# Performance work log

Hardware: AMD Instinct MI355X
Metric: run time of the kernel (lower is better)

## Reference

```python
import jax, jax.numpy as jnp
import numpy as np
from jax import lax

B, L, E, H, VOCAB = 32, 64, 1024, 128, 32000


def setup_inputs() -> dict:
    key = jax.random.key(0)
    ks = jax.random.split(key, 8)
    return {
        "sent": jax.random.randint(ks[0], (B, L), 0, VOCAB),
        "init_c": jax.random.normal(ks[1], (B, H), jnp.float32),
        "init_h": jax.random.normal(ks[2], (B, H), jnp.float32),
        "enc_output": jax.random.normal(ks[3], (B, E, H), jnp.float32),
        "w_emb": jax.random.normal(ks[4], (VOCAB, H), jnp.float32) * 0.02,
        "w_lstm": jax.random.normal(ks[5], (2 * H, 4 * H), jnp.float32) * 0.05,
        "w_soft": jax.random.normal(ks[6], (H, VOCAB), jnp.float32) * 0.05,
        "V": jax.random.normal(ks[7], (2 * H, H), jnp.float32) * 0.05,
    }


def reference(sent, init_c, init_h, enc_output, w_emb, w_lstm, w_soft, V):
    h_dim = init_h.shape[-1]
    x_emb = w_emb[sent]                       # (B, L, H) embedding lookup
    # Split additive-attention matrix: concat(enc, h) @ V == enc @ V_e + h @ V_h
    V_e, V_h = V[:h_dim], V[h_dim:]           # (H, H) each
    enc_proj = enc_output @ V_e               # (B, E, H), precomputed once

    def step(carry, x_t):
        c, h = carry
        # LSTM cell: gates from concat(x, h) @ w_lstm
        gates = jnp.concatenate([x_t, h], axis=-1) @ w_lstm   # (B, 4H)
        i, f, o, g = jnp.split(gates, 4, axis=-1)
        c_new = jax.nn.sigmoid(f) * c + jax.nn.sigmoid(i) * jnp.tanh(g)
        h_new = jax.nn.sigmoid(o) * jnp.tanh(c_new)           # (B, H)
        # Bahdanau additive attention over encoder states
        att = jnp.tanh(enc_proj + (h_new @ V_h)[:, None, :])  # (B, E, H)
        scores = att.sum(axis=-1)                              # (B, E)
        alpha = jax.nn.softmax(scores, axis=-1)                # (B, E)
        context = jnp.einsum('be,beh->bh', alpha, enc_output)  # (B, H)
        h_out = context                                        # attended hidden
        return (c_new, h_out), (h_out, alpha)

    (c_fin, h_fin), (hs, alphas) = lax.scan(step, (init_c, init_h),
                                            jnp.transpose(x_emb, (1, 0, 2)))
    hs = jnp.transpose(hs, (1, 0, 2))          # (B, L, H)
    alphas = jnp.transpose(alphas, (1, 0, 2))  # (B, L, E)
    logits = hs @ w_soft                       # (B, L, vocab)
    return logits, c_fin, h_fin, alphas
```

## Files before the change

### kernel.cpp

```cpp
#include <hip/hip_runtime.h>
#include <hip/hip_bf16.h>

#define BB 32
#define LL 64
#define EE 1024
#define HH 128
#define VV 32000

typedef unsigned short u16;
typedef unsigned long long u64;
typedef __attribute__((ext_vector_type(8))) short bf16x8;
typedef __attribute__((ext_vector_type(4))) float f32x4;

#define LOG2E 1.4426950408889634f
#define C2T   2.8853900817779268f

#define OFF_C ((size_t)BB * LL * VV)
#define OFF_H (OFF_C + (size_t)BB * HH)
#define OFF_A (OFF_H + (size_t)BB * HH)

#define WS_ENCT 0
#define WS_HS   ((size_t)16777216)
#define WS_GX   ((size_t)18350080)
#define WS_PAYU ((size_t)22544384)
#define WS_PAYG ((size_t)23076864)
#define WS_DFL  ((size_t)23339008)
#define WS_NEED ((size_t)23339012)

#define PAYU_WORDS (32 * 8 * 2 * 130)
#define PAYG_WORDS (32 * 8 * 2 * 64)
#define PAY_TOTAL  (PAYU_WORDS + PAYG_WORDS)

__device__ __forceinline__ float bf2f(u16 u) {
    union { unsigned int i; float f; } v; v.i = ((unsigned int)u) << 16; return v.f;
}
__device__ __forceinline__ u16 f2bf(float f) {
    union { float f; unsigned int i; } v; v.f = f;
    unsigned int x = v.i;
    return (u16)((x + 0x7FFFu + ((x >> 16) & 1u)) >> 16);
}
__device__ __forceinline__ float ldf(const void* p, size_t i, int f32) {
    if (f32) return ((const float*)p)[i];
    return bf2f(((const u16*)p)[i]);
}
__device__ __forceinline__ void stout(void* p, size_t i, float v, int f32) {
    if (f32) ((float*)p)[i] = v;
    else ((u16*)p)[i] = f2bf(v);
}
__device__ __forceinline__ float sigm(float x) {
    return __builtin_amdgcn_rcpf(1.f + __builtin_amdgcn_exp2f(-x * LOG2E));
}
__device__ __forceinline__ float tanh_fast(float x) {
    return 1.f - 2.f * __builtin_amdgcn_rcpf(__builtin_amdgcn_exp2f(x * C2T) + 1.f);
}

__global__ __launch_bounds__(256) void resetdetect_kernel(
    u64* __restrict__ pay, const unsigned int* __restrict__ w, int* __restrict__ flag)
{
    int i = blockIdx.x * 256 + threadIdx.x;
    if (i < PAY_TOTAL)
        pay[i] = 0ull;
    if (i == 0) {
        int cnt = 0;
        for (int j = 0; j < 256; ++j) {
            float a = fabsf(bf2f((u16)(w[j] & 0xFFFFu)));
            if (a > 1e-4f && a < 0.5f) ++cnt;
        }
        *flag = (cnt > 128) ? 1 : 0;
    }
}

__global__ __launch_bounds__(256) void gatesx3_kernel(
    const int* __restrict__ sent, const void* __restrict__ w_emb,
    const void* __restrict__ w_lstm, float* __restrict__ gx,
    const int* __restrict__ flagp)
{
    int isf32 = !flagp[0];
    int row0 = blockIdx.x * 16;
    int tid = threadIdx.x;
    __shared__ float xr[16][128];
    for (int i = tid; i < 2048; i += 256) {
        int r = i >> 7, col = i & 127;
        int id = sent[row0 + r];
        xr[r][col] = ldf(w_emb, (size_t)id * HH + col, isf32);
    }
    __syncthreads();
    int c0 = tid, c1 = tid + 256;
    float a0[16], a1[16];
    #pragma unroll
    for (int r = 0; r < 16; ++r) { a0[r] = 0.f; a1[r] = 0.f; }
    for (int kk = 0; kk < 128; ++kk) {
        float w0, w1;
        if (isf32) {
            w0 = ((const float*)w_lstm)[(size_t)kk * 512 + c0];
            w1 = ((const float*)w_lstm)[(size_t)kk * 512 + c1];
        } else {
            w0 = bf2f(((const u16*)w_lstm)[(size_t)kk * 512 + c0]);
            w1 = bf2f(((const u16*)w_lstm)[(size_t)kk * 512 + c1]);
        }
        #pragma unroll
        for (int r = 0; r < 16; ++r) {
            a0[r] += xr[r][kk] * w0;
            a1[r] += xr[r][kk] * w1;
        }
    }
    #pragma unroll
    for (int r = 0; r < 16; ++r) {
        gx[(size_t)(row0 + r) * 512 + c0] = a0[r];
        gx[(size_t)(row0 + r) * 512 + c1] = a1[r];
    }
}

__global__ __launch_bounds__(1024) void transpose_wsoft(
    const void* __restrict__ w_soft, u16* __restrict__ wT, const int* __restrict__ flagp)
{
    int isf32 = !flagp[0];
    __shared__ u16 tile[32][33];
    int n0 = blockIdx.x * 32;
    int k0 = blockIdx.y * 32;
    int tx = threadIdx.x & 31, ty = threadIdx.x >> 5;
    tile[ty][tx] = f2bf(ldf(w_soft, (size_t)(k0 + ty) * VV + n0 + tx, isf32));
    __syncthreads();
    wT[(size_t)(n0 + ty) * HH + k0 + tx] = tile[tx][ty];
}

__global__ __launch_bounds__(256) void encproj_kernel(
    const void* __restrict__ enc_out, const void* __restrict__ V,
    float* __restrict__ encT, const int* __restrict__ flagp)
{
    int isf32 = !flagp[0];
    __shared__ float ve[HH][HH];
    int b = blockIdx.y;
    int e0 = blockIdx.x * 64;
    int tid = threadIdx.x;
    for (int i = tid; i < HH * HH; i += 256)
        ve[i >> 7][i & 127] = ldf(V, i, isf32);
    __syncthreads();
    int e = e0 + (tid & 63);
    int hb = (tid >> 6) * 32;
    size_t rowbase = ((size_t)b * EE + e) * HH;
    float acc[32];
    #pragma unroll
    for (int i = 0; i < 32; ++i) acc[i] = 0.f;
    for (int k0 = 0; k0 < HH; k0 += 16) {
        float ef[16];
        #pragma unroll
        for (int i = 0; i < 16; ++i) ef[i] = ldf(enc_out, rowbase + k0 + i, isf32);
        #pragma unroll
        for (int hh = 0; hh < 32; ++hh) {
            float a = acc[hh];
            #pragma unroll
            for (int kk = 0; kk < 16; ++kk)
                a += ef[kk] * ve[k0 + kk][hb + hh];
            acc[hh] = a;
        }
    }
    float* outp = encT + ((size_t)b * HH) * EE + e;
    #pragma unroll
    for (int hh = 0; hh < 32; ++hh)
        outp[(size_t)(hh + hb) * EE] = acc[hh] * C2T;
}

__global__ __launch_bounds__(1024) void scan_kernel(
    const void* __restrict__ init_c, const void* __restrict__ init_h,
    const void* __restrict__ enc_out, const void* __restrict__ w_lstm,
    const void* __restrict__ V, const float* __restrict__ encTg,
    const float* __restrict__ gx, u16* __restrict__ hs_bf,
    void* __restrict__ out, u64* __restrict__ payu, u64* __restrict__ payg,
    const int* __restrict__ flagp)
{
    const int isf32 = !flagp[0];
    const int bid = blockIdx.x;
    const int b = bid & 31, k = bid >> 5;
    const int tid = threadIdx.x;

    __shared__ u16   encTl16[128][128];
    __shared__ float encF[128][128];
    __shared__ u16   wrec16[64 * 128];
    __shared__ float gall[512];
    __shared__ float harr[128], cst[128], hnew[128], hvC[128];
    __shared__ float dred[8][128];
    __shared__ float sc[128];
    __shared__ float exch[8][130];
    __shared__ float redw[2], redw2[2];
    __shared__ float m_s, s_s;

    for (int i = tid; i < 128 * 128; i += 1024) {
        int h = i >> 7, e = i & 127;
        encTl16[h][e] = f2bf(encTg[(size_t)(b * 128 + h) * EE + k * 128 + e]);
    }
    for (int i = tid; i < 128 * 128; i += 1024) {
        int e = i >> 7, hh = i & 127;
        encF[e][hh] = ldf(enc_out, ((size_t)b * EE + k * 128 + e) * HH + hh, isf32);
    }
    for (int i = tid; i < 64 * 128; i += 1024) {
        int c = i >> 7, kk = i & 127;
        wrec16[c * 128 + kk] = f2bf(ldf(w_lstm, (size_t)(HH + kk) * 512 + k * 64 + c, isf32));
    }
    if (tid < 128) {
        cst[tid]  = ldf(init_c, (size_t)b * HH + tid, isf32);
        harr[tid] = ldf(init_h, (size_t)b * HH + tid, isf32);
    }
    __syncthreads();

    u64* mypu = payu + (size_t)(b * 8 + k) * 2 * 130;
    u64* mypg = payg + (size_t)(b * 8 + k) * 2 * 64;

    for (int t = 0; t < LL; ++t) {
        const unsigned int want = (unsigned int)(t + 1);
        float g0 = 0.f, g1 = 0.f, g2 = 0.f, g3 = 0.f;
        if (tid < 128) {
            const float* gxr = gx + (size_t)(b * LL + t) * 512;
            g0 = gxr[tid]; g1 = gxr[128 + tid]; g2 = gxr[256 + tid]; g3 = gxr[384 + tid];
        }
        {
            int colL = tid >> 4, kc = tid & 15;
            const bf16x8 wv = *(const bf16x8*)&wrec16[colL * 128 + kc * 8];
            float acc = 0.f;
            #pragma unroll
            for (int j = 0; j < 8; ++j)
                acc = __builtin_fmaf(harr[kc * 8 + j], bf2f((u16)wv[j]), acc);
            acc += __shfl_xor(acc, 1);
            acc += __shfl_xor(acc, 2);
            acc += __shfl_xor(acc, 4);
            acc += __shfl_xor(acc, 8);
            if (kc == 0) {
                gall[(k << 6) + colL] = acc;
                union { float f; unsigned int u; } cv; cv.f = acc;
                u64 w = ((u64)want << 32) | (u64)cv.u;
                __hip_atomic_store(&mypg[(size_t)(t & 1) * 64 + colL], w,
                                   __ATOMIC_RELAXED, __HIP_MEMORY_SCOPE_AGENT);
            }
        }
        if (tid < 448) {
            int qq = tid >> 6;
            int q = qq + (qq >= k ? 1 : 0);
            int idx = tid & 63;
            const u64* qp = payg + ((size_t)(b * 8 + q) * 2 + (t & 1)) * 64 + idx;
            u64 w = __hip_atomic_load(qp, __ATOMIC_RELAXED, __HIP_MEMORY_SCOPE_AGENT);
            int cnt = 0;
            while ((unsigned int)(w >> 32) != want) {
                __builtin_amdgcn_s_sleep(1);
                w = __hip_atomic_load(qp, __ATOMIC_RELAXED, __HIP_MEMORY_SCOPE_AGENT);
                if (++cnt > (1 << 20)) break;
            }
            union { unsigned int u; float f; } cv; cv.u = (unsigned int)(w & 0xFFFFFFFFu);
            gall[q * 64 + idx] = cv.f;
        }
        __syncthreads();
        if (tid < 128) {
            float gi = g0 + gall[tid];
            float gf = g1 + gall[128 + tid];
            float go = g2 + gall[256 + tid];
            float gg = g3 + gall[384 + tid];
            float c_new = sigm(gf) * cst[tid] + sigm(gi) * tanh_fast(gg);
            cst[tid] = c_new;
            hnew[tid] = sigm(go) * tanh_fast(c_new);
        }
        __syncthreads();
        {
            int h = tid & 127, jc = tid >> 7;
            float p = 0.f;
            if (isf32) {
                const float* vp = (const float*)V + (size_t)(HH + jc * 16) * HH + h;
                #pragma unroll
                for (int j = 0; j < 16; ++j)
                    p += hnew[jc * 16 + j] * vp[(size_t)j * HH];
            } else {
                const u16* vp = (const u16*)V + (size_t)(HH + jc * 16) * HH + h;
                #pragma unroll
                for (int j = 0; j < 16; ++j)
                    p += hnew[jc * 16 + j] * bf2f(vp[(size_t)j * HH]);
            }
            dred[jc][h] = p;
        }
        __syncthreads();
        if (tid < 128) {
            float v = 0.f;
            #pragma unroll
            for (int s = 0; s < 8; ++s) v += dred[s][tid];
            hvC[tid] = v * C2T;
        }
        __syncthreads();
        {
            int e = tid & 127, hc = tid >> 7;
            float sumr = 0.f;
            #pragma unroll
            for (int j = 0; j < 16; ++j) {
                int h = hc * 16 + j;
                float a = bf2f(encTl16[h][e]) + hvC[h];
                sumr += __builtin_amdgcn_rcpf(__builtin_amdgcn_exp2f(a) + 1.f);
            }
            dred[hc][e] = sumr;
        }
        __syncthreads();
        float s_e = 0.f, p_reg = 0.f;
        if (tid < 128) {
            float sr = 0.f;
            #pragma unroll
            for (int s = 0; s < 8; ++s) sr += dred[s][tid];
            s_e = 128.f - 2.f * sr;
            float m = s_e;
            #pragma unroll
            for (int off = 32; off; off >>= 1) m = fmaxf(m, __shfl_xor(m, off));
            if ((tid & 63) == 0) redw[tid >> 6] = m;
        }
        __syncthreads();
        if (tid < 128) {
            float mloc = fmaxf(redw[0], redw[1]);
            p_reg = __builtin_amdgcn_exp2f((s_e - mloc) * LOG2E);
            sc[tid] = p_reg;
            float s = p_reg;
            #pragma unroll
            for (int off = 32; off; off >>= 1) s += __shfl_xor(s, off);
            if ((tid & 63) == 0) redw2[tid >> 6] = s;
            if (tid == 0) m_s = mloc;
        }
        __syncthreads();
        if (tid == 0) s_s = redw2[0] + redw2[1];
        {
            int h = tid & 127, ec = tid >> 7;
            float p = 0.f;
            #pragma unroll
            for (int j = 0; j < 16; ++j)
                p += sc[ec * 16 + j] * encF[ec * 16 + j][h];
            dred[ec][h] = p;
        }
        __syncthreads();
        float Uv = 0.f;
        if (tid < 128) {
            #pragma unroll
            for (int s = 0; s < 8; ++s) Uv += dred[s][tid];
        }
        {
            u64* pp = mypu + (size_t)(t & 1) * 130;
            if (tid < 130) {
                float val = (tid < 128) ? Uv : ((tid == 128) ? m_s : s_s);
                union { float f; unsigned int u; } cv; cv.f = val;
                u64 w = ((u64)want << 32) | (u64)cv.u;
                __hip_atomic_store(&pp[tid], w, __ATOMIC_RELAXED, __HIP_MEMORY_SCOPE_AGENT);
                exch[k][tid] = val;
            }
        }
        if (tid < 910) {
            int qq = tid / 130;
            int q = qq + (qq >= k ? 1 : 0);
            int idx = tid - qq * 130;
            const u64* qp = payu + ((size_t)(b * 8 + q) * 2 + (t & 1)) * 130 + idx;
            u64 w = __hip_atomic_load(qp, __ATOMIC_RELAXED, __HIP_MEMORY_SCOPE_AGENT);
            int cnt = 0;
            while ((unsigned int)(w >> 32) != want) {
                __builtin_amdgcn_s_sleep(1);
                w = __hip_atomic_load(qp, __ATOMIC_RELAXED, __HIP_MEMORY_SCOPE_AGENT);
                if (++cnt > (1 << 20)) break;
            }
            union { unsigned int u; float f; } cv; cv.u = (unsigned int)(w & 0xFFFFFFFFu);
            exch[q][idx] = cv.f;
        }
        __syncthreads();
        if (tid < 128) {
            float M = exch[0][128];
            #pragma unroll
            for (int q = 1; q < 8; ++q) M = fmaxf(M, exch[q][128]);
            float St = 0.f, ch = 0.f;
            #pragma unroll
            for (int q = 0; q < 8; ++q) {
                float w = __builtin_amdgcn_exp2f((exch[q][128] - M) * LOG2E);
                St += w * exch[q][129];
                ch += w * exch[q][tid];
            }
            float rS = __builtin_amdgcn_rcpf(St);
            float ctx = ch * rS;
            harr[tid] = ctx;
            float al = p_reg * __builtin_amdgcn_exp2f((m_s - M) * LOG2E) * rS;
            stout(out, OFF_A + (size_t)(b * LL + t) * EE + k * 128 + tid, al, isf32);
            if (k == 0) {
                hs_bf[(size_t)(b * LL + t) * HH + tid] = f2bf(ctx);
                if (t == LL - 1) {
                    stout(out, OFF_H + (size_t)b * HH + tid, ctx, isf32);
                    stout(out, OFF_C + (size_t)b * HH + tid, cst[tid], isf32);
                }
            }
        }
        __syncthreads();
    }
}

__global__ __launch_bounds__(256) void logits_gemm(
    const u16* __restrict__ hs, const u16* __restrict__ wT,
    void* __restrict__ out, const int* __restrict__ flagp)
{
    int isf32 = !flagp[0];
    int n0 = blockIdx.x * 32;
    int m0 = (blockIdx.y * 4 + (threadIdx.x >> 6)) * 32;
    int lane = threadIdx.x & 63;
    int lr = lane & 15, lh = lane >> 4;
    f32x4 acc00 = {0.f, 0.f, 0.f, 0.f}, acc01 = acc00, acc10 = acc00, acc11 = acc00;
    const u16* a0p = hs + (size_t)(m0 + lr) * HH + lh * 8;
    const u16* a1p = a0p + (size_t)16 * HH;
    const u16* b0p = wT + (size_t)(n0 + lr) * HH + lh * 8;
    const u16* b1p = b0p + (size_t)16 * HH;
    #pragma unroll
    for (int ks = 0; ks < 4; ++ks) {
        bf16x8 a0 = *(const bf16x8*)(a0p + ks * 32);
        bf16x8 a1 = *(const bf16x8*)(a1p + ks * 32);
        bf16x8 b0 = *(const bf16x8*)(b0p + ks * 32);
        bf16x8 b1 = *(const bf16x8*)(b1p + ks * 32);
        acc00 = __builtin_amdgcn_mfma_f32_16x16x32_bf16(a0, b0, acc00, 0, 0, 0);
        acc01 = __builtin_amdgcn_mfma_f32_16x16x32_bf16(a0, b1, acc01, 0, 0, 0);
        acc10 = __builtin_amdgcn_mfma_f32_16x16x32_bf16(a1, b0, acc10, 0, 0, 0);
        acc11 = __builtin_amdgcn_mfma_f32_16x16x32_bf16(a1, b1, acc11, 0, 0, 0);
    }
    size_t base0 = (size_t)(m0 + lh * 4) * VV + n0;
    size_t base1 = (size_t)(m0 + 16 + lh * 4) * VV + n0;
    #pragma unroll
    for (int r = 0; r < 4; ++r) {
        stout(out, base0 + (size_t)r * VV + lr,      acc00[r], isf32);
        stout(out, base0 + (size_t)r * VV + 16 + lr, acc01[r], isf32);
        stout(out, base1 + (size_t)r * VV + lr,      acc10[r], isf32);
        stout(out, base1 + (size_t)r * VV + 16 + lr, acc11[r], isf32);
    }
}

extern "C" void kernel_launch(void* const* d_in, const int* in_sizes, int n_in,
                              void* d_out, int out_size, void* d_ws, size_t ws_size,
                              hipStream_t stream)
{
    (void)in_sizes; (void)n_in; (void)out_size;
    if (ws_size < WS_NEED) return;

    const int* sent     = (const int*)d_in[0];
    const void* init_c  = d_in[1];
    const void* init_h  = d_in[2];
    const void* enc_out = d_in[3];
    const void* w_emb   = d_in[4];
    const void* w_lstm  = d_in[5];
    const void* w_soft  = d_in[6];
    const void* V       = d_in[7];

    char* ws = (char*)d_ws;
    float* encT  = (float*)(ws + WS_ENCT);
    u16*   wT    = (u16*)(ws + WS_ENCT);
    u16*   hs    = (u16*)(ws + WS_HS);
    float* gx    = (float*)(ws + WS_GX);
    u64*   payu  = (u64*)(ws + WS_PAYU);
    u64*   payg  = (u64*)(ws + WS_PAYG);
    int*   dflag = (int*)(ws + WS_DFL);

    hipLaunchKernelGGL(resetdetect_kernel, dim3((PAY_TOTAL + 255) / 256), dim3(256), 0, stream,
                       payu, (const unsigned int*)w_emb, dflag);
    hipLaunchKernelGGL(gatesx3_kernel, dim3(128), dim3(256), 0, stream,
                       sent, w_emb, w_lstm, gx, dflag);
    hipLaunchKernelGGL(encproj_kernel, dim3(16, BB), dim3(256), 0, stream, enc_out, V, encT, dflag);

    {
        const void* a0 = init_c; const void* a1 = init_h; const void* a2 = enc_out;
        const void* a3 = w_lstm; const void* a4 = V; const float* a5 = encT;
        const float* a6 = gx; u16* a7 = hs; void* a8 = d_out;
        u64* a9 = payu; u64* a10 = payg; const int* a11 = dflag;
        void* args[] = {&a0, &a1, &a2, &a3, &a4, &a5, &a6, &a7, &a8, &a9, &a10, &a11};
        hipLaunchCooperativeKernel(scan_kernel, dim3(256), dim3(1024), args, 0, stream);
    }

    hipLaunchKernelGGL(transpose_wsoft, dim3(VV / 32, 4), dim3(1024), 0, stream, w_soft, wT, dflag);
    hipLaunchKernelGGL(logits_gemm, dim3(VV / 32, 16), dim3(256), 0, stream, hs, wT, d_out, dflag);
}
```

Measured before the change: 775.9 us.

## Merge prep kernels into one launch and cache V_h in LDS for scan

Folds the payload reset, dtype detection, input-gate GEMM, encoder projection and w_soft transpose into one megaprep kernel with block-range dispatch, moving the transpose ahead of the scan into its own workspace region. The encoder projection is now stored as bf16, halving its workspace traffic and the scan's load. The scan caches V_h in shared memory as bf16 instead of reading it from global memory every step. It also replaces the two-stage dred reductions with LDS atomicAdd, trading a barrier for atomic contention. The extra LDS use may push against the shared memory limit, and the atomic accumulation order is nondeterministic.

```diff
diff --git a/kernel.cpp b/kernel.cpp
--- a/kernel.cpp
+++ b/kernel.cpp
@@ -10,6 +10,7 @@
 typedef unsigned short u16;
 typedef unsigned long long u64;
 typedef __attribute__((ext_vector_type(8))) short bf16x8;
+typedef __attribute__((ext_vector_type(8))) unsigned short u16x8;
 typedef __attribute__((ext_vector_type(4))) float f32x4;
 
 #define LOG2E 1.4426950408889634f
@@ -20,16 +21,23 @@
 #define OFF_A (OFF_H + (size_t)BB * HH)
 
 #define WS_ENCT 0
-#define WS_HS   ((size_t)16777216)
-#define WS_GX   ((size_t)18350080)
-#define WS_PAYU ((size_t)22544384)
-#define WS_PAYG ((size_t)23076864)
-#define WS_DFL  ((size_t)23339008)
-#define WS_NEED ((size_t)23339012)
+#define WS_HS   ((size_t)8388608)
+#define WS_GX   ((size_t)8912896)
+#define WS_PAYU ((size_t)13107200)
+#define WS_PAYG ((size_t)13639680)
+#define WS_WT   ((size_t)13901824)
+#define WS_DFL  ((size_t)22093824)
+#define WS_NEED ((size_t)22093828)
 
 #define PAYU_WORDS (32 * 8 * 2 * 130)
 #define PAYG_WORDS (32 * 8 * 2 * 64)
 #define PAY_TOTAL  (PAYU_WORDS + PAYG_WORDS)
+
+#define RESET_BLKS ((PAY_TOTAL + 255) / 256)
+#define GX_BLKS    128
+#define ENC_BLKS   (16 * BB)
+#define TW_BLKS    ((VV / 32) * 4)
+#define PREP_BLKS  (RESET_BLKS + GX_BLKS + ENC_BLKS + TW_BLKS)
 
 __device__ __forceinline__ float bf2f(u16 u) {
     union { unsigned int i; float f; } v; v.i = ((unsigned int)u) << 16; return v.f;
@@ -54,117 +62,130 @@
     return 1.f - 2.f * __builtin_amdgcn_rcpf(__builtin_amdgcn_exp2f(x * C2T) + 1.f);
 }
 
-__global__ __launch_bounds__(256) void resetdetect_kernel(
-    u64* __restrict__ pay, const unsigned int* __restrict__ w, int* __restrict__ flag)
+__global__ __launch_bounds__(256) void megaprep_kernel(
+    const int* __restrict__ sent, const void* __restrict__ w_emb,
+    const void* __restrict__ w_lstm, const void* __restrict__ enc_out,
+    const void* __restrict__ V, const void* __restrict__ w_soft,
+    float* __restrict__ gx, u16* __restrict__ encT, u16* __restrict__ wT,
+    u64* __restrict__ pay, int* __restrict__ flag)
 {
-    int i = blockIdx.x * 256 + threadIdx.x;
-    if (i < PAY_TOTAL)
-        pay[i] = 0ull;
-    if (i == 0) {
-        int cnt = 0;
-        for (int j = 0; j < 256; ++j) {
-            float a = fabsf(bf2f((u16)(w[j] & 0xFFFFu)));
-            if (a > 1e-4f && a < 0.5f) ++cnt;
-        }
-        *flag = (cnt > 128) ? 1 : 0;
-    }
-}
-
-__global__ __launch_bounds__(256) void gatesx3_kernel(
-    const int* __restrict__ sent, const void* __restrict__ w_emb,
-    const void* __restrict__ w_lstm, float* __restrict__ gx,
-    const int* __restrict__ flagp)
-{
-    int isf32 = !flagp[0];
-    int row0 = blockIdx.x * 16;
-    int tid = threadIdx.x;
-    __shared__ float xr[16][128];
-    for (int i = tid; i < 2048; i += 256) {
-        int r = i >> 7, col = i & 127;
-        int id = sent[row0 + r];
-        xr[r][col] = ldf(w_emb, (size_t)id * HH + col, isf32);
-    }
+    const int blk = blockIdx.x;
+    const int tid = threadIdx.x;
+    __shared__ float smem[16384];
+    __shared__ int dcnt[4];
+
+    if (blk < RESET_BLKS) {
+        int i = blk * 256 + tid;
+        if (i < PAY_TOTAL) pay[i] = 0ull;
+        if (blk == 0) {
+            float a = fabsf(bf2f((u16)(((const unsigned int*)w_emb)[tid] & 0xFFFFu)));
+            unsigned long long m = __ballot(a > 1e-4f && a < 0.5f);
+            if ((tid & 63) == 0) dcnt[tid >> 6] = __popcll(m);
+            __syncthreads();
+            if (tid == 0)
+                *flag = (dcnt[0] + dcnt[1] + dcnt[2] + dcnt[3] > 128) ? 1 : 0;
+        }
+        return;
+    }
+    float da = fabsf(bf2f((u16)(((const unsigned int*)w_emb)[tid] & 0xFFFFu)));
+    unsigned long long dm = __ballot(da > 1e-4f && da < 0.5f);
+    if ((tid & 63) == 0) dcnt[tid >> 6] = __popcll(dm);
     __syncthreads();
-    int c0 = tid, c1 = tid + 256;
-    float a0[16], a1[16];
-    #pragma unroll
-    for (int r = 0; r < 16; ++r) { a0[r] = 0.f; a1[r] = 0.f; }
-    for (int kk = 0; kk < 128; ++kk) {
-        float w0, w1;
-        if (isf32) {
-            w0 = ((const float*)w_lstm)[(size_t)kk * 512 + c0];
-            w1 = ((const float*)w_lstm)[(size_t)kk * 512 + c1];
-        } else {
-            w0 = bf2f(((const u16*)w_lstm)[(size_t)kk * 512 + c0]);
-            w1 = bf2f(((const u16*)w_lstm)[(size_t)kk * 512 + c1]);
+    const int isf32 = !(dcnt[0] + dcnt[1] + dcnt[2] + dcnt[3] > 128);
+    __syncthreads();
+
+    if (blk < RESET_BLKS + GX_BLKS) {
+        int row0 = (blk - RESET_BLKS) * 16;
+        float (*xr)[128] = (float(*)[128])smem;
+        for (int i = tid; i < 2048; i += 256) {
+            int r = i >> 7, col = i & 127;
+            int id = sent[row0 + r];
+            xr[r][col] = ldf(w_emb, (size_t)id * HH + col, isf32);
+        }
+        __syncthreads();
+        int c0 = tid, c1 = tid + 256;
+        float a0[16], a1[16];
+        #pragma unroll
+        for (int r = 0; r < 16; ++r) { a0[r] = 0.f; a1[r] = 0.f; }
+        for (int kk = 0; kk < 128; ++kk) {
+            float w0, w1;
+            if (isf32) {
+                w0 = ((const float*)w_lstm)[(size_t)kk * 512 + c0];
+                w1 = ((const float*)w_lstm)[(size_t)kk * 512 + c1];
+            } else {
+                w0 = bf2f(((const u16*)w_lstm)[(size_t)kk * 512 + c0]);
+                w1 = bf2f(((const u16*)w_lstm)[(size_t)kk * 512 + c1]);
+            }
+            #pragma unroll
+            for (int r = 0; r < 16; ++r) {
+                a0[r] += xr[r][kk] * w0;
+                a1[r] += xr[r][kk] * w1;
+            }
         }
         #pragma unroll
         for (int r = 0; r < 16; ++r) {
-            a0[r] += xr[r][kk] * w0;
-            a1[r] += xr[r][kk] * w1;
-        }
-    }
-    #pragma unroll
-    for (int r = 0; r < 16; ++r) {
-        gx[(size_t)(row0 + r) * 512 + c0] = a0[r];
-        gx[(size_t)(row0 + r) * 512 + c1] = a1[r];
-    }
-}
-
-__global__ __launch_bounds__(1024) void transpose_wsoft(
-    const void* __restrict__ w_soft, u16* __restrict__ wT, const int* __restrict__ flagp)
-{
-    int isf32 = !flagp[0];
-    __shared__ u16 tile[32][33];
-    int n0 = blockIdx.x * 32;
-    int k0 = blockIdx.y * 32;
-    int tx = threadIdx.x & 31, ty = threadIdx.x >> 5;
-    tile[ty][tx] = f2bf(ldf(w_soft, (size_t)(k0 + ty) * VV + n0 + tx, isf32));
-    __syncthreads();
-    wT[(size_t)(n0 + ty) * HH + k0 + tx] = tile[tx][ty];
-}
-
-__global__ __launch_bounds__(256) void encproj_kernel(
-    const void* __restrict__ enc_out, const void* __restrict__ V,
-    float* __restrict__ encT, const int* __restrict__ flagp)
-{
-    int isf32 = !flagp[0];
-    __shared__ float ve[HH][HH];
-    int b = blockIdx.y;
-    int e0 = blockIdx.x * 64;
-    int tid = threadIdx.x;
-    for (int i = tid; i < HH * HH; i += 256)
-        ve[i >> 7][i & 127] = ldf(V, i, isf32);
-    __syncthreads();
-    int e = e0 + (tid & 63);
-    int hb = (tid >> 6) * 32;
-    size_t rowbase = ((size_t)b * EE + e) * HH;
-    float acc[32];
-    #pragma unroll
-    for (int i = 0; i < 32; ++i) acc[i] = 0.f;
-    for (int k0 = 0; k0 < HH; k0 += 16) {
-        float ef[16];
-        #pragma unroll
-        for (int i = 0; i < 16; ++i) ef[i] = ldf(enc_out, rowbase + k0 + i, isf32);
-        #pragma unroll
-        for (int hh = 0; hh < 32; ++hh) {
-            float a = acc[hh];
-            #pragma unroll
-            for (int kk = 0; kk < 16; ++kk)
-                a += ef[kk] * ve[k0 + kk][hb + hh];
-            acc[hh] = a;
-        }
-    }
-    float* outp = encT + ((size_t)b * HH) * EE + e;
-    #pragma unroll
-    for (int hh = 0; hh < 32; ++hh)
-        outp[(size_t)(hh + hb) * EE] = acc[hh] * C2T;
+            gx[(size_t)(row0 + r) * 512 + c0] = a0[r];
+            gx[(size_t)(row0 + r) * 512 + c1] = a1[r];
+        }
+        return;
+    }
+    if (blk < RESET_BLKS + GX_BLKS + ENC_BLKS) {
+        int idx = blk - RESET_BLKS - GX_BLKS;
+        int b = idx >> 4;
+        int e0 = (idx & 15) * 64;
+        float (*ve)[128] = (float(*)[128])smem;
+        for (int i = tid; i < HH * HH; i += 256)
+            ve[i >> 7][i & 127] = ldf(V, i, isf32);
+        __syncthreads();
+        int e = e0 + (tid & 63);
+        int hb = (tid >> 6) * 32;
+        size_t rowbase = ((size_t)b * EE + e) * HH;
+        float acc[32];
+        #pragma unroll
+        for (int i = 0; i < 32; ++i) acc[i] = 0.f;
+        for (int k0 = 0; k0 < HH; k0 += 16) {
+            float ef[16];
+            #pragma unroll
+            for (int i = 0; i < 16; ++i) ef[i] = ldf(enc_out, rowbase + k0 + i, isf32);
+            #pragma unroll
+            for (int hh = 0; hh < 32; ++hh) {
+                float a = acc[hh];
+                #pragma unroll
+                for (int kk = 0; kk < 16; ++kk)
+                    a += ef[kk] * ve[k0 + kk][hb + hh];
+                acc[hh] = a;
+            }
+        }
+        u16* outp = encT + ((size_t)b * HH) * EE + e;
+        #pragma unroll
+        for (int hh = 0; hh < 32; ++hh)
+            outp[(size_t)(hh + hb) * EE] = f2bf(acc[hh] * C2T);
+        return;
+    }
+    {
+        int idx = blk - RESET_BLKS - GX_BLKS - ENC_BLKS;
+        int n0 = (idx >> 2) * 32;
+        int k0 = (idx & 3) * 32;
+        u16 (*tile)[33] = (u16(*)[33])smem;
+        int tx = tid & 31, ty0 = tid >> 5;
+        #pragma unroll
+        for (int i = 0; i < 4; ++i) {
+            int ty = ty0 + i * 8;
+            tile[ty][tx] = f2bf(ldf(w_soft, (size_t)(k0 + ty) * VV + n0 + tx, isf32));
+        }
+        __syncthreads();
+        #pragma unroll
+        for (int i = 0; i < 4; ++i) {
+            int ty = ty0 + i * 8;
+            wT[(size_t)(n0 + ty) * HH + k0 + tx] = tile[tx][ty];
+        }
+    }
 }
 
 __global__ __launch_bounds__(1024) void scan_kernel(
     const void* __restrict__ init_c, const void* __restrict__ init_h,
     const void* __restrict__ enc_out, const void* __restrict__ w_lstm,
-    const void* __restrict__ V, const float* __restrict__ encTg,
+    const void* __restrict__ V, const u16* __restrict__ encTg16,
     const float* __restrict__ gx, u16* __restrict__ hs_bf,
     void* __restrict__ out, u64* __restrict__ payu, u64* __restrict__ payg,
     const int* __restrict__ flagp)
@@ -177,21 +198,26 @@
     __shared__ u16   encTl16[128][128];
     __shared__ float encF[128][128];
     __shared__ u16   wrec16[64 * 128];
-    __shared__ float gall[512];
-    __shared__ float harr[128], cst[128], hnew[128], hvC[128];
+    __shared__ u16   vhl[128][128];
     __shared__ float dred[8][128];
+    __shared__ float harr[128], cst[128], hnew[128], hvC[128], Ul[128];
     __shared__ float sc[128];
     __shared__ float exch[8][130];
     __shared__ float redw[2], redw2[2];
     __shared__ float m_s, s_s;
+    float* gall = &dred[0][0];
 
     for (int i = tid; i < 128 * 128; i += 1024) {
         int h = i >> 7, e = i & 127;
-        encTl16[h][e] = f2bf(encTg[(size_t)(b * 128 + h) * EE + k * 128 + e]);
+        encTl16[h][e] = encTg16[(size_t)(b * 128 + h) * EE + k * 128 + e];
     }
     for (int i = tid; i < 128 * 128; i += 1024) {
         int e = i >> 7, hh = i & 127;
         encF[e][hh] = ldf(enc_out, ((size_t)b * EE + k * 128 + e) * HH + hh, isf32);
+    }
+    for (int i = tid; i < 128 * 128; i += 1024) {
+        int j = i >> 7, h = i & 127;
+        vhl[j][h] = f2bf(ldf(V, (size_t)(HH + j) * HH + h, isf32));
     }
     for (int i = tid; i < 64 * 128; i += 1024) {
         int c = i >> 7, kk = i & 127;
@@ -227,8 +253,8 @@
             if (kc == 0) {
                 gall[(k << 6) + colL] = acc;
                 union { float f; unsigned int u; } cv; cv.f = acc;
-                u64 w = ((u64)want << 32) | (u64)cv.u;
-                __hip_atomic_store(&mypg[(size_t)(t & 1) * 64 + colL], w,
+                u64 wd = ((u64)want << 32) | (u64)cv.u;
+                __hip_atomic_store(&mypg[(size_t)(t & 1) * 64 + colL], wd,
                                    __ATOMIC_RELAXED, __HIP_MEMORY_SCOPE_AGENT);
             }
         }
@@ -237,14 +263,14 @@
             int q = qq + (qq >= k ? 1 : 0);
             int idx = tid & 63;
             const u64* qp = payg + ((size_t)(b * 8 + q) * 2 + (t & 1)) * 64 + idx;
-            u64 w = __hip_atomic_load(qp, __ATOMIC_RELAXED, __HIP_MEMORY_SCOPE_AGENT);
+            u64 wd = __hip_atomic_load(qp, __ATOMIC_RELAXED, __HIP_MEMORY_SCOPE_AGENT);
             int cnt = 0;
-            while ((unsigned int)(w >> 32) != want) {
+            while ((unsigned int)(wd >> 32) != want) {
                 __builtin_amdgcn_s_sleep(1);
-                w = __hip_atomic_load(qp, __ATOMIC_RELAXED, __HIP_MEMORY_SCOPE_AGENT);
+                wd = __hip_atomic_load(qp, __ATOMIC_RELAXED, __HIP_MEMORY_SCOPE_AGENT);
                 if (++cnt > (1 << 20)) break;
             }
-            union { unsigned int u; float f; } cv; cv.u = (unsigned int)(w & 0xFFFFFFFFu);
+            union { unsigned int u; float f; } cv; cv.u = (unsigned int)(wd & 0xFFFFFFFFu);
             gall[q * 64 + idx] = cv.f;
         }
         __syncthreads();
@@ -256,30 +282,17 @@
             float c_new = sigm(gf) * cst[tid] + sigm(gi) * tanh_fast(gg);
             cst[tid] = c_new;
             hnew[tid] = sigm(go) * tanh_fast(c_new);
+        } else if (tid < 256) {
+            hvC[tid - 128] = 0.f;
         }
         __syncthreads();
         {
             int h = tid & 127, jc = tid >> 7;
             float p = 0.f;
-            if (isf32) {
-                const float* vp = (const float*)V + (size_t)(HH + jc * 16) * HH + h;
-                #pragma unroll
-                for (int j = 0; j < 16; ++j)
-                    p += hnew[jc * 16 + j] * vp[(size_t)j * HH];
-            } else {
-                const u16* vp = (const u16*)V + (size_t)(HH + jc * 16) * HH + h;
-                #pragma unroll
-                for (int j = 0; j < 16; ++j)
-                    p += hnew[jc * 16 + j] * bf2f(vp[(size_t)j * HH]);
-            }
-            dred[jc][h] = p;
-        }
-        __syncthreads();
-        if (tid < 128) {
-            float v = 0.f;
-            #pragma unroll
-            for (int s = 0; s < 8; ++s) v += dred[s][tid];
-            hvC[tid] = v * C2T;
+            #pragma unroll
+            for (int j = 0; j < 16; ++j)
+                p = __builtin_fmaf(hnew[jc * 16 + j], bf2f(vhl[jc * 16 + j][h]), p);
+            atomicAdd(&hvC[h], p * C2T);
         }
         __syncthreads();
         {
@@ -304,6 +317,8 @@
             #pragma unroll
             for (int off = 32; off; off >>= 1) m = fmaxf(m, __shfl_xor(m, off));
             if ((tid & 63) == 0) redw[tid >> 6] = m;
+        } else if (tid < 256) {
+            Ul[tid - 128] = 0.f;
         }
         __syncthreads();
         if (tid < 128) {
@@ -323,22 +338,17 @@
             float p = 0.f;
             #pragma unroll
             for (int j = 0; j < 16; ++j)
-                p += sc[ec * 16 + j] * encF[ec * 16 + j][h];
-            dred[ec][h] = p;
-        }
-        __syncthreads();
-        float Uv = 0.f;
-        if (tid < 128) {
-            #pragma unroll
-            for (int s = 0; s < 8; ++s) Uv += dred[s][tid];
-        }
+                p = __builtin_fmaf(sc[ec * 16 + j], encF[ec * 16 + j][h], p);
+            atomicAdd(&Ul[h], p);
+        }
+        __syncthreads();
         {
             u64* pp = mypu + (size_t)(t & 1) * 130;
             if (tid < 130) {
-                float val = (tid < 128) ? Uv : ((tid == 128) ? m_s : s_s);
+                float val = (tid < 128) ? Ul[tid] : ((tid == 128) ? m_s : s_s);
                 union { float f; unsigned int u; } cv; cv.f = val;
-                u64 w = ((u64)want << 32) | (u64)cv.u;
-                __hip_atomic_store(&pp[tid], w, __ATOMIC_RELAXED, __HIP_MEMORY_SCOPE_AGENT);
+                u64 wd = ((u64)want << 32) | (u64)cv.u;
+                __hip_atomic_store(&pp[tid], wd, __ATOMIC_RELAXED, __HIP_MEMORY_SCOPE_AGENT);
                 exch[k][tid] = val;
             }
         }
@@ -347,14 +357,14 @@
             int q = qq + (qq >= k ? 1 : 0);
             int idx = tid - qq * 130;
             const u64* qp = payu + ((size_t)(b * 8 + q) * 2 + (t & 1)) * 130 + idx;
-            u64 w = __hip_atomic_load(qp, __ATOMIC_RELAXED, __HIP_MEMORY_SCOPE_AGENT);
+            u64 wd = __hip_atomic_load(qp, __ATOMIC_RELAXED, __HIP_MEMORY_SCOPE_AGENT);
             int cnt = 0;
-            while ((unsigned int)(w >> 32) != want) {
+            while ((unsigned int)(wd >> 32) != want) {
                 __builtin_amdgcn_s_sleep(1);
-                w = __hip_atomic_load(qp, __ATOMIC_RELAXED, __HIP_MEMORY_SCOPE_AGENT);
+                wd = __hip_atomic_load(qp, __ATOMIC_RELAXED, __HIP_MEMORY_SCOPE_AGENT);
                 if (++cnt > (1 << 20)) break;
             }
-            union { unsigned int u; float f; } cv; cv.u = (unsigned int)(w & 0xFFFFFFFFu);
+            union { unsigned int u; float f; } cv; cv.u = (unsigned int)(wd & 0xFFFFFFFFu);
             exch[q][idx] = cv.f;
         }
         __syncthreads();
@@ -365,9 +375,9 @@
             float St = 0.f, ch = 0.f;
             #pragma unroll
             for (int q = 0; q < 8; ++q) {
-                float w = __builtin_amdgcn_exp2f((exch[q][128] - M) * LOG2E);
-                St += w * exch[q][129];
-                ch += w * exch[q][tid];
+                float wq = __builtin_amdgcn_exp2f((exch[q][128] - M) * LOG2E);
+                St += wq * exch[q][129];
+                ch += wq * exch[q][tid];
             }
             float rS = __builtin_amdgcn_rcpf(St);
             float ctx = ch * rS;
@@ -439,29 +449,26 @@
     const void* V       = d_in[7];
 
     char* ws = (char*)d_ws;
-    float* encT  = (float*)(ws + WS_ENCT);
-    u16*   wT    = (u16*)(ws + WS_ENCT);
+    u16*   encT  = (u16*)(ws + WS_ENCT);
     u16*   hs    = (u16*)(ws + WS_HS);
     float* gx    = (float*)(ws + WS_GX);
     u64*   payu  = (u64*)(ws + WS_PAYU);
     u64*   payg  = (u64*)(ws + WS_PAYG);
+    u16*   wT    = (u16*)(ws + WS_WT);
     int*   dflag = (int*)(ws + WS_DFL);
 
-    hipLaunchKernelGGL(resetdetect_kernel, dim3((PAY_TOTAL + 255) / 256), dim3(256), 0, stream,
-                       payu, (const unsigned int*)w_emb, dflag);
-    hipLaunchKernelGGL(gatesx3_kernel, dim3(128), dim3(256), 0, stream,
-                       sent, w_emb, w_lstm, gx, dflag);
-    hipLaunchKernelGGL(encproj_kernel, dim3(16, BB), dim3(256), 0, stream, enc_out, V, encT, dflag);
+    hipLaunchKernelGGL(megaprep_kernel, dim3(PREP_BLKS), dim3(256), 0, stream,
+                       sent, w_emb, w_lstm, enc_out, V, w_soft,
+                       gx, encT, wT, payu, dflag);
 
     {
         const void* a0 = init_c; const void* a1 = init_h; const void* a2 = enc_out;
-        const void* a3 = w_lstm; const void* a4 = V; const float* a5 = encT;
+        const void* a3 = w_lstm; const void* a4 = V; const u16* a5 = encT;
         const float* a6 = gx; u16* a7 = hs; void* a8 = d_out;
         u64* a9 = payu; u64* a10 = payg; const int* a11 = dflag;
         void* args[] = {&a0, &a1, &a2, &a3, &a4, &a5, &a6, &a7, &a8, &a9, &a10, &a11};
         hipLaunchCooperativeKernel(scan_kernel, dim3(256), dim3(1024), args, 0, stream);
     }
 
-    hipLaunchKernelGGL(transpose_wsoft, dim3(VV / 32, 4), dim3(1024), 0, stream, w_soft, wT, dflag);
     hipLaunchKernelGGL(logits_gemm, dim3(VV / 32, 16), dim3(256), 0, stream, hs, wT, d_out, dflag);
 }
```

Result: slower. 879.9 us (+13.4%).
